# Performance work log

Measured on AMD Instinct MI355X. Metric: run time of the kernel, lower is better.

The kernel has to match this reference:

```python
import jax, jax.numpy as jnp
import numpy as np

N = 16384

def setup_inputs() -> dict:
    key = jax.random.key(0)
    k1, k2 = jax.random.split(key)
    inputs = jax.random.normal(k1, (N,), dtype=jnp.float32)
    targets = jax.random.randint(k2, (N,), 0, 2)  # int, values in {0,1}
    return {"inputs": inputs, "targets": targets}

def reference(inputs, targets):
    # Flatten, split logits into positives (targets==1) and negatives (targets==0).
    x = inputs.reshape(-1)
    t = targets.reshape(-1).astype(jnp.float32)
    pos_mask = (t == 1.0).astype(x.dtype)  # (N,)
    neg_mask = (t == 0.0).astype(x.dtype)  # (N,)
    # BCE-with-logits against target=1 on diff = x_i - x_j is softplus(-diff).
    # Masked full NxN formulation (jit-friendly, same math as pos/neg outer diff).
    diff = x[:, None] - x[None, :]                      # (N, N)
    pair_w = pos_mask[:, None] * neg_mask[None, :]      # 1 for (pos, neg) pairs
    loss_sum = jnp.sum(jax.nn.softplus(-diff) * pair_w)
    n_pairs = jnp.sum(pair_w)
    # Original returns 0.0 if no pos or no neg examples.
    return jnp.where(n_pairs > 0, loss_sum / jnp.maximum(n_pairs, 1.0), 0.0)
```

## Files before the change

kernel.cpp:

```cpp
#include <hip/hip_runtime.h>


#define PT   512
#define RB   32
#define CAP  16384

template<int NQ>
__device__ __forceinline__ float row_stream(const float* __restrict__ lds_en,
                                            const float* __restrict__ lds_emp,
                                            int nf4, int tid) {
    float emp[NQ * 8];
#pragma unroll
    for (int r = 0; r < NQ * 8; ++r) emp[r] = lds_emp[r];
    float acc[NQ];
#pragma unroll
    for (int q = 0; q < NQ; ++q) acc[q] = 0.f;

    auto do_col = [&](float en) {
#pragma unroll
        for (int q = 0; q < NQ; ++q) {
            float p0 = __builtin_fmaf(en, emp[q * 8 + 0], 1.f);
            p0 *= __builtin_fmaf(en, emp[q * 8 + 1], 1.f);
            p0 *= __builtin_fmaf(en, emp[q * 8 + 2], 1.f);
            p0 *= __builtin_fmaf(en, emp[q * 8 + 3], 1.f);
            float p1 = __builtin_fmaf(en, emp[q * 8 + 4], 1.f);
            p1 *= __builtin_fmaf(en, emp[q * 8 + 5], 1.f);
            p1 *= __builtin_fmaf(en, emp[q * 8 + 6], 1.f);
            p1 *= __builtin_fmaf(en, emp[q * 8 + 7], 1.f);
            acc[q] += __log2f(p0 * p1);
        }
    };

    const float4* __restrict__ en4 = (const float4*)lds_en;
#pragma unroll 2
    for (int v = tid; v < nf4; v += PT) {
        const float4 e4 = en4[v];
        do_col(e4.x);
        do_col(e4.y);
        do_col(e4.z);
        do_col(e4.w);
    }
    float s = 0.f;
#pragma unroll
    for (int q = 0; q < NQ; ++q) s += acc[q];
    return s;
}

__global__ __launch_bounds__(PT, 4)
void pair_local(const float* __restrict__ x, const int* __restrict__ tg, int n,
                double* __restrict__ partials) {
    __shared__ float  lds_en[CAP];
    __shared__ float  lds_emp[RB];
    __shared__ int    lds_k;
    __shared__ int    swsum[PT / 64], swoff[PT / 64], stot;
    __shared__ double wsum[PT / 64];
    const int bid = blockIdx.x, tid = threadIdx.x;
    const int lane = tid & 63, wid = tid >> 6;
    const int n4 = n >> 2;

    if (wid == 0) {
        float ex = 0.f; int isp = 0;
        const int row = bid * RB + lane;
        if (lane < RB && row < n) {
            isp = (tg[row] == 1);
            if (isp) ex = __expf(-x[row]);
        }
        const unsigned long long m = __ballot(isp);
        if (lane < RB) lds_emp[lane] = 0.f;
        const int rank = (int)__popcll(m & ((1ull << lane) - 1ull));
        if (isp) lds_emp[rank] = ex;
        if (lane == 0) lds_k = (int)__popcll(m);
    }

    float4 xv4[8]; unsigned negmask = 0;
    int cn = 0;
#pragma unroll
    for (int k = 0; k < 8; ++k) {
        const int v = tid + (k << 9);
        float4 xq = make_float4(0, 0, 0, 0);
        int4   tq = make_int4(-1, -1, -1, -1);
        if (v < n4) { xq = ((const float4*)x)[v]; tq = ((const int4*)tg)[v]; }
        xv4[k] = xq;
        cn += (tq.x == 0) + (tq.y == 0) + (tq.z == 0) + (tq.w == 0);
        negmask |= (unsigned)(tq.x == 0) << (4 * k + 0);
        negmask |= (unsigned)(tq.y == 0) << (4 * k + 1);
        negmask |= (unsigned)(tq.z == 0) << (4 * k + 2);
        negmask |= (unsigned)(tq.w == 0) << (4 * k + 3);
    }

    int inc = cn;
#pragma unroll
    for (int off = 1; off < 64; off <<= 1) {
        int u = __shfl_up(inc, off, 64);
        if (lane >= off) inc += u;
    }
    if (lane == 63) swsum[wid] = inc;
    __syncthreads();
    if (tid < 8) {
        int val = swsum[tid];
        int sc = val;
#pragma unroll
        for (int off = 1; off < 8; off <<= 1) {
            int u = __shfl_up(sc, off, 64);
            if (tid >= off) sc += u;
        }
        swoff[tid] = sc - val;
        if (tid == 7) stot = sc;
    }
    __syncthreads();
    const int nn = stot;
    const int kq = (lds_k + 7) >> 3;
    int idx = swoff[wid] + (inc - cn);

    const int lim4 = (nn + 3) >> 2;
    for (int i = nn + tid; i < (lim4 << 2); i += PT) lds_en[i] = 0.f;
#define STEP(V, B)                                        \
    if ((negmask >> (B)) & 1u) lds_en[idx++] = __expf(V);
#pragma unroll
    for (int k = 0; k < 8; ++k) {
        STEP(xv4[k].x, 4 * k + 0)
        STEP(xv4[k].y, 4 * k + 1)
        STEP(xv4[k].z, 4 * k + 2)
        STEP(xv4[k].w, 4 * k + 3)
    }
#undef STEP
    __syncthreads();

    float s = 0.f;
    if (kq == 1)      s = row_stream<1>(lds_en, lds_emp, lim4, tid);
    else if (kq == 2) s = row_stream<2>(lds_en, lds_emp, lim4, tid);
    else if (kq == 3) s = row_stream<3>(lds_en, lds_emp, lim4, tid);
    else if (kq >= 4) s = row_stream<4>(lds_en, lds_emp, lim4, tid);

#pragma unroll
    for (int off = 32; off > 0; off >>= 1) s += __shfl_down(s, off, 64);
    if (lane == 0) wsum[wid] = (double)s;
    __syncthreads();
    if (tid == 0) {
        double b = 0.0;
#pragma unroll
        for (int w = 0; w < PT / 64; ++w) b += wsum[w];
        partials[bid] = b;
    }
}

__global__ __launch_bounds__(1024)
void finalize_kernel(const int* __restrict__ tg, int n,
                     const double* __restrict__ partials, int nb,
                     float* __restrict__ out) {
    const int tid = threadIdx.x;
    int cp = 0, cn = 0;
    const int4* t4 = (const int4*)tg;
    for (int v = tid; v < (n >> 2); v += 1024) {
        const int4 t = t4[v];
        cp += (t.x == 1) + (t.y == 1) + (t.z == 1) + (t.w == 1);
        cn += (t.x == 0) + (t.y == 0) + (t.z == 0) + (t.w == 0);
    }
    double d = 0.0;
    for (int k = tid; k < nb; k += 1024) d += partials[k];
    int c = cp | (cn << 16);
#pragma unroll
    for (int off = 32; off > 0; off >>= 1) {
        d += __shfl_down(d, off, 64);
        c += __shfl_down(c, off, 64);
    }
    __shared__ double fs[16];
    __shared__ int    fc[16];
    if ((tid & 63) == 0) { fs[tid >> 6] = d; fc[tid >> 6] = c; }
    __syncthreads();
    if (tid == 0) {
        double ssum = 0.0; int tot = 0;
#pragma unroll
        for (int w = 0; w < 16; ++w) { ssum += fs[w]; tot += fc[w]; }
        const int np = tot & 0xffff, nn = tot >> 16;
        const double npairs = (double)np * (double)nn;
        out[0] = (npairs > 0.0) ? (float)(ssum * 0.6931471805599453 / npairs) : 0.0f;
    }
}

extern "C" void kernel_launch(void* const* d_in, const int* in_sizes, int n_in,
                              void* d_out, int out_size, void* d_ws, size_t ws_size,
                              hipStream_t stream) {
    const float* x  = (const float*)d_in[0];
    const int*   tg = (const int*)d_in[1];
    const int n = in_sizes[0];

    double* partials = (double*)d_ws;
    const int nblocks = (n + RB - 1) / RB;

    pair_local<<<nblocks, PT, 0, stream>>>(x, tg, n, partials);
    finalize_kernel<<<1, 1024, 0, stream>>>(tg, n, partials, nblocks, (float*)d_out);
}
```

Baseline: 18.87 us.

## Drop negative compaction, double rows per block, move count to pair kernel

Each block now writes exp(x) for all elements into LDS, with positives zeroed, instead of prefix-scanning and compacting only the negatives. The full array is then streamed; zero entries contribute log(1)=0. Rows per block go from 32 to 64 (up to 8 quads), which halves the grid. Negative counts are computed per block and the finalize kernel shrinks to one wave reading the counts. This removes the scans and two barriers but roughly doubles the streamed columns per row, since non-negatives are no longer skipped.

After: 20.31 us. +7.6%, slower.

```diff
diff --git a/kernel.cpp b/kernel.cpp
--- a/kernel.cpp
+++ b/kernel.cpp
@@ -2,8 +2,8 @@
 
 
 #define PT   512
-#define RB   32
-#define CAP  16384
+#define RB   64
+#define NB   256
 
 template<int NQ>
 __device__ __forceinline__ float row_stream(const float* __restrict__ lds_en,
@@ -48,133 +48,91 @@
 
 __global__ __launch_bounds__(PT, 4)
 void pair_local(const float* __restrict__ x, const int* __restrict__ tg, int n,
-                double* __restrict__ partials) {
-    __shared__ float  lds_en[CAP];
+                double* __restrict__ partials, int* __restrict__ cnts) {
+    __shared__ float  lds_en[16384];
     __shared__ float  lds_emp[RB];
     __shared__ int    lds_k;
-    __shared__ int    swsum[PT / 64], swoff[PT / 64], stot;
     __shared__ double wsum[PT / 64];
+    __shared__ int    wcnt[PT / 64];
     const int bid = blockIdx.x, tid = threadIdx.x;
     const int lane = tid & 63, wid = tid >> 6;
     const int n4 = n >> 2;
 
     if (wid == 0) {
+        const int row = bid * RB + lane;
         float ex = 0.f; int isp = 0;
-        const int row = bid * RB + lane;
-        if (lane < RB && row < n) {
+        if (row < n) {
             isp = (tg[row] == 1);
             if (isp) ex = __expf(-x[row]);
         }
         const unsigned long long m = __ballot(isp);
-        if (lane < RB) lds_emp[lane] = 0.f;
+        lds_emp[lane] = 0.f;
         const int rank = (int)__popcll(m & ((1ull << lane) - 1ull));
         if (isp) lds_emp[rank] = ex;
         if (lane == 0) lds_k = (int)__popcll(m);
     }
 
-    float4 xv4[8]; unsigned negmask = 0;
     int cn = 0;
 #pragma unroll
     for (int k = 0; k < 8; ++k) {
         const int v = tid + (k << 9);
-        float4 xq = make_float4(0, 0, 0, 0);
-        int4   tq = make_int4(-1, -1, -1, -1);
-        if (v < n4) { xq = ((const float4*)x)[v]; tq = ((const int4*)tg)[v]; }
-        xv4[k] = xq;
-        cn += (tq.x == 0) + (tq.y == 0) + (tq.z == 0) + (tq.w == 0);
-        negmask |= (unsigned)(tq.x == 0) << (4 * k + 0);
-        negmask |= (unsigned)(tq.y == 0) << (4 * k + 1);
-        negmask |= (unsigned)(tq.z == 0) << (4 * k + 2);
-        negmask |= (unsigned)(tq.w == 0) << (4 * k + 3);
+        float4 e = make_float4(0.f, 0.f, 0.f, 0.f);
+        if (v < n4) {
+            const float4 xq = ((const float4*)x)[v];
+            const int4   tq = ((const int4*)tg)[v];
+            e.x = (tq.x == 0) ? __expf(xq.x) : 0.f;
+            e.y = (tq.y == 0) ? __expf(xq.y) : 0.f;
+            e.z = (tq.z == 0) ? __expf(xq.z) : 0.f;
+            e.w = (tq.w == 0) ? __expf(xq.w) : 0.f;
+            cn += (tq.x == 0) + (tq.y == 0) + (tq.z == 0) + (tq.w == 0);
+        }
+        ((float4*)lds_en)[v] = e;
+    }
+    __syncthreads();
+
+    const int kq = (lds_k + 7) >> 3;
+    float s = 0.f;
+    switch (kq) {
+        case 0: break;
+        case 1: s = row_stream<1>(lds_en, lds_emp, n4, tid); break;
+        case 2: s = row_stream<2>(lds_en, lds_emp, n4, tid); break;
+        case 3: s = row_stream<3>(lds_en, lds_emp, n4, tid); break;
+        case 4: s = row_stream<4>(lds_en, lds_emp, n4, tid); break;
+        case 5: s = row_stream<5>(lds_en, lds_emp, n4, tid); break;
+        case 6: s = row_stream<6>(lds_en, lds_emp, n4, tid); break;
+        case 7: s = row_stream<7>(lds_en, lds_emp, n4, tid); break;
+        default: s = row_stream<8>(lds_en, lds_emp, n4, tid); break;
     }
 
-    int inc = cn;
 #pragma unroll
-    for (int off = 1; off < 64; off <<= 1) {
-        int u = __shfl_up(inc, off, 64);
-        if (lane >= off) inc += u;
+    for (int off = 32; off > 0; off >>= 1) {
+        s  += __shfl_down(s, off, 64);
+        cn += __shfl_down(cn, off, 64);
     }
-    if (lane == 63) swsum[wid] = inc;
-    __syncthreads();
-    if (tid < 8) {
-        int val = swsum[tid];
-        int sc = val;
-#pragma unroll
-        for (int off = 1; off < 8; off <<= 1) {
-            int u = __shfl_up(sc, off, 64);
-            if (tid >= off) sc += u;
-        }
-        swoff[tid] = sc - val;
-        if (tid == 7) stot = sc;
-    }
-    __syncthreads();
-    const int nn = stot;
-    const int kq = (lds_k + 7) >> 3;
-    int idx = swoff[wid] + (inc - cn);
-
-    const int lim4 = (nn + 3) >> 2;
-    for (int i = nn + tid; i < (lim4 << 2); i += PT) lds_en[i] = 0.f;
-#define STEP(V, B)                                        \
-    if ((negmask >> (B)) & 1u) lds_en[idx++] = __expf(V);
-#pragma unroll
-    for (int k = 0; k < 8; ++k) {
-        STEP(xv4[k].x, 4 * k + 0)
-        STEP(xv4[k].y, 4 * k + 1)
-        STEP(xv4[k].z, 4 * k + 2)
-        STEP(xv4[k].w, 4 * k + 3)
-    }
-#undef STEP
-    __syncthreads();
-
-    float s = 0.f;
-    if (kq == 1)      s = row_stream<1>(lds_en, lds_emp, lim4, tid);
-    else if (kq == 2) s = row_stream<2>(lds_en, lds_emp, lim4, tid);
-    else if (kq == 3) s = row_stream<3>(lds_en, lds_emp, lim4, tid);
-    else if (kq >= 4) s = row_stream<4>(lds_en, lds_emp, lim4, tid);
-
-#pragma unroll
-    for (int off = 32; off > 0; off >>= 1) s += __shfl_down(s, off, 64);
-    if (lane == 0) wsum[wid] = (double)s;
+    if (lane == 0) { wsum[wid] = (double)s; wcnt[wid] = cn; }
     __syncthreads();
     if (tid == 0) {
-        double b = 0.0;
+        double b = 0.0; int t = 0;
 #pragma unroll
-        for (int w = 0; w < PT / 64; ++w) b += wsum[w];
+        for (int w = 0; w < PT / 64; ++w) { b += wsum[w]; t += wcnt[w]; }
         partials[bid] = b;
+        cnts[bid] = t;
     }
 }
 
-__global__ __launch_bounds__(1024)
-void finalize_kernel(const int* __restrict__ tg, int n,
-                     const double* __restrict__ partials, int nb,
-                     float* __restrict__ out) {
-    const int tid = threadIdx.x;
-    int cp = 0, cn = 0;
-    const int4* t4 = (const int4*)tg;
-    for (int v = tid; v < (n >> 2); v += 1024) {
-        const int4 t = t4[v];
-        cp += (t.x == 1) + (t.y == 1) + (t.z == 1) + (t.w == 1);
-        cn += (t.x == 0) + (t.y == 0) + (t.z == 0) + (t.w == 0);
-    }
+__global__ __launch_bounds__(64)
+void finalize_kernel(const double* __restrict__ partials, const int* __restrict__ cnts,
+                     int nb, int n, float* __restrict__ out) {
+    const int lane = threadIdx.x;
     double d = 0.0;
-    for (int k = tid; k < nb; k += 1024) d += partials[k];
-    int c = cp | (cn << 16);
+    for (int k = lane; k < nb; k += 64) d += partials[k];
 #pragma unroll
-    for (int off = 32; off > 0; off >>= 1) {
-        d += __shfl_down(d, off, 64);
-        c += __shfl_down(c, off, 64);
-    }
-    __shared__ double fs[16];
-    __shared__ int    fc[16];
-    if ((tid & 63) == 0) { fs[tid >> 6] = d; fc[tid >> 6] = c; }
-    __syncthreads();
-    if (tid == 0) {
-        double ssum = 0.0; int tot = 0;
-#pragma unroll
-        for (int w = 0; w < 16; ++w) { ssum += fs[w]; tot += fc[w]; }
-        const int np = tot & 0xffff, nn = tot >> 16;
+    for (int off = 32; off > 0; off >>= 1) d += __shfl_down(d, off, 64);
+    if (lane == 0) {
+        const int nn = cnts[0];
+        const int np = n - nn;
         const double npairs = (double)np * (double)nn;
-        out[0] = (npairs > 0.0) ? (float)(ssum * 0.6931471805599453 / npairs) : 0.0f;
+        out[0] = (npairs > 0.0) ? (float)(d * 0.6931471805599453 / npairs) : 0.0f;
     }
 }
 
@@ -185,9 +143,11 @@
     const int*   tg = (const int*)d_in[1];
     const int n = in_sizes[0];
 
-    double* partials = (double*)d_ws;
+    char* ws = (char*)d_ws;
+    double* partials = (double*)(ws);
+    int*    cnts     = (int*)(ws + 4096);
+
     const int nblocks = (n + RB - 1) / RB;
-
-    pair_local<<<nblocks, PT, 0, stream>>>(x, tg, n, partials);
-    finalize_kernel<<<1, 1024, 0, stream>>>(tg, n, partials, nblocks, (float*)d_out);
+    pair_local<<<nblocks, PT, 0, stream>>>(x, tg, n, partials, cnts);
+    finalize_kernel<<<1, 64, 0, stream>>>(partials, cnts, nblocks, n, (float*)d_out);
 }
```
